# Performance work log

Hardware: AMD Instinct MI355X
Metric: run time of the kernel (lower is better)

Reference implementation:

```python
import jax, jax.numpy as jnp
import numpy as np

B, DIN, DOUT = 8192, 4096, 4096
BIAS_OFFSET = 512.0


def setup_inputs() -> dict:
    key = jax.random.key(0)
    kx, kw = jax.random.split(key)
    x = jax.random.normal(kx, (B, DIN), dtype=jnp.float32)
    # Ternary weights in {-1, 0, 1}, iid with zero_prob=0.5 and mean 0:
    # P(0)=0.5, P(-1)=P(1)=0.25
    u = jax.random.uniform(kw, (DIN, DOUT))
    W = jnp.where(u < 0.25, -1.0, jnp.where(u < 0.5, 1.0, 0.0)).astype(jnp.float32)
    b = jnp.full((DOUT,), BIAS_OFFSET, dtype=jnp.float32)
    return {"x": x, "W": W, "b": b}


def reference(x, W, b):
    # z: pre-activation of ternary-weight linear layer  [B, DOUT]
    z = jnp.matmul(x, W) + b
    # binarized activation (sign with ties -> +1), as in TernBin forward
    x_out = jnp.where(z >= 0, 1.0, -1.0).astype(z.dtype)
    return (x_out, z)
```

## Files before the change

### kernel.cpp

```cpp
#include <hip/hip_runtime.h>
#include <stdint.h>

#define MDIM 8192
#define NDIM 4096
#define KDIM 4096

#define BM 256
#define BN 256
#define BK 64
#define NT (KDIM / BK)

#define CVT_X_BLOCKS 16384
#define CVT_W_BLOCKS 4096

typedef __bf16 bf16x8 __attribute__((ext_vector_type(8)));
typedef float f32x4 __attribute__((ext_vector_type(4)));

#define GPTR(p) ((const __attribute__((address_space(1))) void*)(p))
#define LPTR(p) ((__attribute__((address_space(3))) void*)(p))

#define BAR() asm volatile("s_barrier" ::: "memory")

__device__ __forceinline__ uint32_t f2bf(float f) {
  union { float f; uint32_t u; } c; c.f = f;
  uint32_t u = c.u;
  u += 0x7fffu + ((u >> 16) & 1u);
  return u >> 16;
}

__global__ __launch_bounds__(256) void cvt_fused(const float* __restrict__ x,
                                                 const float* __restrict__ W,
                                                 unsigned short* __restrict__ xb,
                                                 unsigned short* __restrict__ Wt) {
  __shared__ uint32_t T[64][37];
  const int bid = blockIdx.x;
  const int t = threadIdx.x;
  if (bid < CVT_X_BLOCKS) {
    size_t i = ((size_t)bid * 256 + t) * 8;
    const float4* p = (const float4*)(x + i);
    float4 a = p[0], b = p[1];
    uint4 r;
    r.x = f2bf(a.x) | (f2bf(a.y) << 16);
    r.y = f2bf(a.z) | (f2bf(a.w) << 16);
    r.z = f2bf(b.x) | (f2bf(b.y) << 16);
    r.w = f2bf(b.z) | (f2bf(b.w) << 16);
    *(uint4*)(xb + i) = r;
  } else {
    const int wb = bid - CVT_X_BLOCKS;
    const int n0 = (wb & 63) * 64;
    const int k0 = (wb >> 6) * 64;
    const int nl = t & 63;
    const int kpb = t >> 6;
#pragma unroll
    for (int i = 0; i < 8; ++i) {
      int kp = kpb + 4 * i;
      int k = 2 * kp;
      float v0 = W[(size_t)(k0 + k) * NDIM + n0 + nl];
      float v1 = W[(size_t)(k0 + k + 1) * NDIM + n0 + nl];
      T[nl][kp] = f2bf(v0) | (f2bf(v1) << 16);
    }
    __syncthreads();
    const int ch = t & 7;
    const int nb = t >> 3;
#pragma unroll
    for (int h = 0; h < 2; ++h) {
      int n = nb + 32 * h;
      uint4 v;
      v.x = T[n][ch * 4 + 0];
      v.y = T[n][ch * 4 + 1];
      v.z = T[n][ch * 4 + 2];
      v.w = T[n][ch * 4 + 3];
      *(uint4*)&Wt[(size_t)(n0 + n) * KDIM + k0 + ch * 8] = v;
    }
  }
}


__device__ __forceinline__ void stage2(unsigned short* dst,
                                       const unsigned short* G, int half,
                                       int tile, int wave) {
#pragma unroll
  for (int i = 0; i < 2; ++i) {
    const int rb = half * 128 + i * 64;
    __builtin_amdgcn_global_load_lds(
        GPTR(G + (size_t)rb * KDIM + (size_t)tile * 64),
        LPTR(dst + (rb + wave * 8) * BK), 16, 0, 0);
  }
}

template <int IB>
__device__ __forceinline__ void load_a4(const unsigned short* buf, int wm,
                                        int rA, int k0off, int k1off,
                                        bf16x8 (&a)[4][2]) {
#pragma unroll
  for (int i = 0; i < 4; ++i) {
    const unsigned short* p = buf + (size_t)(wm * 128 + (IB + i) * 16 + rA) * BK;
    a[i][0] = *(const bf16x8*)(p + k0off);
    a[i][1] = *(const bf16x8*)(p + k1off);
  }
}

template <int JB>
__device__ __forceinline__ void load_b2(const unsigned short* buf, int wn,
                                        int rA, int k0off, int k1off,
                                        bf16x8 (&b)[4][2]) {
#pragma unroll
  for (int j = 0; j < 2; ++j) {
    const unsigned short* p = buf + (size_t)(wn * 64 + (JB + j) * 16 + rA) * BK;
    b[JB + j][0] = *(const bf16x8*)(p + k0off);
    b[JB + j][1] = *(const bf16x8*)(p + k1off);
  }
}

template <int IB, int JB>
__device__ __forceinline__ void mfma16(const bf16x8 (&a)[4][2],
                                       const bf16x8 (&b)[4][2],
                                       f32x4 (&acc)[8][4]) {
  __builtin_amdgcn_s_setprio(1);
#pragma unroll
  for (int i = 0; i < 4; ++i)
#pragma unroll
    for (int j = 0; j < 2; ++j)
#pragma unroll
      for (int kk = 0; kk < 2; ++kk)
        acc[IB + i][JB + j] = __builtin_amdgcn_mfma_f32_16x16x32_bf16(
            b[JB + j][kk], a[i][kk], acc[IB + i][JB + j], 0, 0, 0);
  __builtin_amdgcn_s_setprio(0);
}

template <bool SA, bool SB, int VM>
__device__ __forceinline__ void tile_step(
    const unsigned short* curA, const unsigned short* curB,
    unsigned short* nxtA, unsigned short* stageB, int T,
    const unsigned short* Ag, const unsigned short* Bg, int wave, int wm,
    int wn, int rA, int k0off, int k1off, bf16x8 (&a)[4][2], bf16x8 (&b)[4][2],
    f32x4 (&acc)[8][4]) {
  load_a4<0>(curA, wm, rA, k0off, k1off, a);
  load_b2<0>(curB, wn, rA, k0off, k1off, b);
  if (SA) stage2(nxtA, Ag, 0, T + 1, wave);
  BAR();
  mfma16<0, 0>(a, b, acc);
  BAR();
  load_b2<2>(curB, wn, rA, k0off, k1off, b);
  if (SA) stage2(nxtA, Ag, 1, T + 1, wave);
  BAR();
  mfma16<0, 2>(a, b, acc);
  BAR();
  load_a4<4>(curA, wm, rA, k0off, k1off, a);
  if (SB) stage2(stageB, Bg, 0, T + 2, wave);
  BAR();
  mfma16<4, 0>(a, b, acc);
  BAR();
  if (SB) stage2(stageB, Bg, 1, T + 2, wave);
  if constexpr (VM == 4) asm volatile("s_waitcnt vmcnt(4)" ::: "memory");
  else if constexpr (VM == 0) asm volatile("s_waitcnt vmcnt(0)" ::: "memory");
  BAR();
  mfma16<4, 2>(a, b, acc);
  BAR();
}

__global__ __launch_bounds__(512, 2) void gemm_bf16_8ph(
    const unsigned short* __restrict__ Ab, const unsigned short* __restrict__ Bt,
    const float* __restrict__ bias, float* __restrict__ out) {
  __shared__ __align__(16) unsigned short lds[4 * BM * BK];
  unsigned short* A0 = lds;
  unsigned short* B0 = lds + 1 * BM * BK;
  unsigned short* A1 = lds + 2 * BM * BK;
  unsigned short* B1 = lds + 3 * BM * BK;

  const int tid = threadIdx.x;
  const int lane = tid & 63;
  const int wave = tid >> 6;
  const int wm = wave & 1;
  const int wn = wave >> 1;

  const int bid = blockIdx.x;
  const int wg = (bid & 7) * 64 + (bid >> 3);
  const int m0 = (wg >> 4) * BM;
  const int n0 = (wg & 15) * BN;

  f32x4 acc[8][4];
#pragma unroll
  for (int i = 0; i < 8; ++i)
#pragma unroll
    for (int j = 0; j < 4; ++j) {
      f32x4 z = {0.0f, 0.0f, 0.0f, 0.0f};
      acc[i][j] = z;
    }

  const int tr = tid >> 3;
  const int tc = (tid & 7) ^ (tr & 7);
  const unsigned short* Ag = Ab + (size_t)(m0 + tr) * KDIM + tc * 8;
  const unsigned short* Bg = Bt + (size_t)(n0 + tr) * KDIM + tc * 8;

  const int rA = lane & 15;
  const int hi = lane >> 4;
  const int key = lane & 7;
  const int k0off = ((0 + hi) ^ key) * 8;
  const int k1off = ((4 + hi) ^ key) * 8;

  bf16x8 a[4][2], b[4][2];

  stage2(B0, Bg, 0, 0, wave);
  stage2(B0, Bg, 1, 0, wave);
  stage2(A0, Ag, 0, 0, wave);
  stage2(A0, Ag, 1, 0, wave);
  stage2(B1, Bg, 0, 1, wave);
  stage2(B1, Bg, 1, 1, wave);
  asm volatile("s_waitcnt vmcnt(4)" ::: "memory");
  BAR();

  for (int T = 0; T < NT - 2; T += 2) {
    tile_step<true, true, 4>(A0, B0, A1, B0, T, Ag, Bg, wave, wm, wn, rA,
                             k0off, k1off, a, b, acc);
    tile_step<true, true, 4>(A1, B1, A0, B1, T + 1, Ag, Bg, wave, wm, wn, rA,
                             k0off, k1off, a, b, acc);
  }
  tile_step<true, false, 0>(A0, B0, A1, B0, NT - 2, Ag, Bg, wave, wm, wn, rA,
                            k0off, k1off, a, b, acc);
  tile_step<false, false, -1>(A1, B1, A0, B1, NT - 1, Ag, Bg, wave, wm, wn, rA,
                              k0off, k1off, a, b, acc);

  float* zout = out + (size_t)MDIM * NDIM;
  const int ml = lane & 15;
  const int nb4 = (lane >> 4) * 4;
#pragma unroll
  for (int i = 0; i < 8; ++i) {
    int m = m0 + wm * 128 + i * 16 + ml;
    float* zrow = zout + (size_t)m * NDIM;
    float* srow = out + (size_t)m * NDIM;
#pragma unroll
    for (int j = 0; j < 4; ++j) {
      int n = n0 + wn * 64 + j * 16 + nb4;
      float4 bv = *(const float4*)&bias[n];
      f32x4 v = acc[i][j];
      float4 z, s;
      z.x = v[0] + bv.x; z.y = v[1] + bv.y; z.z = v[2] + bv.z; z.w = v[3] + bv.w;
      s.x = (z.x >= 0.0f) ? 1.0f : -1.0f;
      s.y = (z.y >= 0.0f) ? 1.0f : -1.0f;
      s.z = (z.z >= 0.0f) ? 1.0f : -1.0f;
      s.w = (z.w >= 0.0f) ? 1.0f : -1.0f;
      *(float4*)&zrow[n] = z;
      *(float4*)&srow[n] = s;
    }
  }
}

__device__ __forceinline__ void mfma_step128(const unsigned short* As,
                                             const unsigned short* Bs,
                                             f32x4 acc[4][4], int lane, int wm,
                                             int wn) {
  const int rA = lane & 15;
  const int key = lane & 7;
#pragma unroll
  for (int kk = 0; kk < 2; ++kk) {
    const int koff = ((kk * 4 + (lane >> 4)) ^ key) * 8;
    bf16x8 a[4], b[4];
#pragma unroll
    for (int i = 0; i < 4; ++i) {
      a[i] = *(const bf16x8*)(As + (size_t)(wm * 64 + i * 16 + rA) * 64 + koff);
      b[i] = *(const bf16x8*)(Bs + (size_t)(wn * 64 + i * 16 + rA) * 64 + koff);
    }
#pragma unroll
    for (int i = 0; i < 4; ++i)
#pragma unroll
      for (int j = 0; j < 4; ++j)
        acc[i][j] = __builtin_amdgcn_mfma_f32_16x16x32_bf16(b[j], a[i],
                                                            acc[i][j], 0, 0, 0);
  }
}

__global__ __launch_bounds__(256) void gemm_bf16_nows(
    const float* __restrict__ x, const float* __restrict__ W,
    const float* __restrict__ bias, float* __restrict__ out) {
  __shared__ __align__(16) unsigned short As[128 * 64];
  __shared__ __align__(16) unsigned short Bs[128 * 64];

  const int tid = threadIdx.x;
  const int lane = tid & 63;
  const int wave = tid >> 6;
  const int wm = wave & 1;
  const int wn = wave >> 1;
  const int m0 = blockIdx.y * 128;
  const int n0 = blockIdx.x * 128;

  f32x4 acc[4][4];
#pragma unroll
  for (int i = 0; i < 4; ++i)
#pragma unroll
    for (int j = 0; j < 4; ++j) {
      f32x4 z = {0.0f, 0.0f, 0.0f, 0.0f};
      acc[i][j] = z;
    }

  for (int k0 = 0; k0 < KDIM; k0 += 64) {
    {
      const int kc = (tid & 15) * 4;
      const int cb = kc >> 3;
      const int wi = kc & 7;
      const int rowb = tid >> 4;
#pragma unroll
      for (int r = 0; r < 8; ++r) {
        int row = rowb + 16 * r;
        float4 v = *(const float4*)&x[(size_t)(m0 + row) * KDIM + k0 + kc];
        uint2 pk;
        pk.x = f2bf(v.x) | (f2bf(v.y) << 16);
        pk.y = f2bf(v.z) | (f2bf(v.w) << 16);
        *(uint2*)&As[row * 64 + ((cb ^ (row & 7)) * 8) + wi] = pk;
      }
    }
    {
      const int nc = (tid & 31) * 4;
      const int kb = tid >> 5;
#pragma unroll
      for (int r = 0; r < 8; ++r) {
        int krow = kb + 8 * r;
        int cb = krow >> 3, wi = krow & 7;
        float4 v = *(const float4*)&W[(size_t)(k0 + krow) * NDIM + n0 + nc];
        Bs[(nc + 0) * 64 + ((cb ^ ((nc + 0) & 7)) * 8) + wi] = (unsigned short)f2bf(v.x);
        Bs[(nc + 1) * 64 + ((cb ^ ((nc + 1) & 7)) * 8) + wi] = (unsigned short)f2bf(v.y);
        Bs[(nc + 2) * 64 + ((cb ^ ((nc + 2) & 7)) * 8) + wi] = (unsigned short)f2bf(v.z);
        Bs[(nc + 3) * 64 + ((cb ^ ((nc + 3) & 7)) * 8) + wi] = (unsigned short)f2bf(v.w);
      }
    }
    __syncthreads();
    mfma_step128(As, Bs, acc, lane, wm, wn);
    __syncthreads();
  }

  float* zout = out + (size_t)MDIM * NDIM;
  const int ml = lane & 15;
  const int nb4 = (lane >> 4) * 4;
#pragma unroll
  for (int i = 0; i < 4; ++i) {
    int m = m0 + wm * 64 + i * 16 + ml;
    float* zrow = zout + (size_t)m * NDIM;
    float* srow = out + (size_t)m * NDIM;
#pragma unroll
    for (int j = 0; j < 4; ++j) {
      int n = n0 + wn * 64 + j * 16 + nb4;
      float4 bv = *(const float4*)&bias[n];
      f32x4 v = acc[i][j];
      float4 z, s;
      z.x = v[0] + bv.x; z.y = v[1] + bv.y; z.z = v[2] + bv.z; z.w = v[3] + bv.w;
      s.x = (z.x >= 0.0f) ? 1.0f : -1.0f;
      s.y = (z.y >= 0.0f) ? 1.0f : -1.0f;
      s.z = (z.z >= 0.0f) ? 1.0f : -1.0f;
      s.w = (z.w >= 0.0f) ? 1.0f : -1.0f;
      *(float4*)&zrow[n] = z;
      *(float4*)&srow[n] = s;
    }
  }
}

extern "C" void kernel_launch(void* const* d_in, const int* in_sizes, int n_in,
                              void* d_out, int out_size, void* d_ws,
                              size_t ws_size, hipStream_t stream) {
  (void)in_sizes; (void)n_in; (void)out_size;
  const float* x = (const float*)d_in[0];
  const float* W = (const float*)d_in[1];
  const float* b = (const float*)d_in[2];
  float* out = (float*)d_out;

  const size_t xb_elems = (size_t)MDIM * KDIM;
  const size_t wt_elems = (size_t)KDIM * NDIM;
  const size_t need = (xb_elems + wt_elems) * sizeof(unsigned short);

  if (ws_size >= need) {
    unsigned short* xb = (unsigned short*)d_ws;
    unsigned short* wt = xb + xb_elems;
    cvt_fused<<<CVT_X_BLOCKS + CVT_W_BLOCKS, 256, 0, stream>>>(x, W, xb, wt);
    gemm_bf16_8ph<<<(MDIM / BM) * (NDIM / BN), 512, 0, stream>>>(xb, wt, b, out);
  } else {
    dim3 fgrid(NDIM / 128, MDIM / 128);
    gemm_bf16_nows<<<fgrid, 256, 0, stream>>>(x, W, b, out);
  }
}
```

Measured before the change: 602.2 us.

## Fuse fp32-to-bf16 conversion of x into GEMM A-tile loading

Drops the separate pass that converted x to bf16 in workspace. The GEMM now loads fp32 x into registers, converts it with packed bf16 conversion instructions, and writes swizzled tiles to LDS within the pipeline. This removes the pre-pass write and re-read of a 64MB intermediate. In exchange, the GEMM reads fp32 A, which doubles the A bytes per tile, and holds extra staging registers.

Result: slower. 778.2 us (+29.2%).

```diff
diff --git a/kernel.cpp b/kernel.cpp
--- a/kernel.cpp
+++ b/kernel.cpp
@@ -10,7 +10,6 @@
 #define BK 64
 #define NT (KDIM / BK)
 
-#define CVT_X_BLOCKS 16384
 #define CVT_W_BLOCKS 4096
 
 typedef __bf16 bf16x8 __attribute__((ext_vector_type(8)));
@@ -28,50 +27,41 @@
   return u >> 16;
 }
 
-__global__ __launch_bounds__(256) void cvt_fused(const float* __restrict__ x,
-                                                 const float* __restrict__ W,
-                                                 unsigned short* __restrict__ xb,
-                                                 unsigned short* __restrict__ Wt) {
+__device__ __forceinline__ uint32_t cvtpk(float lo, float hi) {
+  uint32_t r;
+  asm("v_cvt_pk_bf16_f32 %0, %1, %2" : "=v"(r) : "v"(lo), "v"(hi));
+  return r;
+}
+
+__global__ __launch_bounds__(256) void cvt_w(const float* __restrict__ W,
+                                             unsigned short* __restrict__ Wt) {
   __shared__ uint32_t T[64][37];
-  const int bid = blockIdx.x;
+  const int wb = blockIdx.x;
   const int t = threadIdx.x;
-  if (bid < CVT_X_BLOCKS) {
-    size_t i = ((size_t)bid * 256 + t) * 8;
-    const float4* p = (const float4*)(x + i);
-    float4 a = p[0], b = p[1];
-    uint4 r;
-    r.x = f2bf(a.x) | (f2bf(a.y) << 16);
-    r.y = f2bf(a.z) | (f2bf(a.w) << 16);
-    r.z = f2bf(b.x) | (f2bf(b.y) << 16);
-    r.w = f2bf(b.z) | (f2bf(b.w) << 16);
-    *(uint4*)(xb + i) = r;
-  } else {
-    const int wb = bid - CVT_X_BLOCKS;
-    const int n0 = (wb & 63) * 64;
-    const int k0 = (wb >> 6) * 64;
-    const int nl = t & 63;
-    const int kpb = t >> 6;
-#pragma unroll
-    for (int i = 0; i < 8; ++i) {
-      int kp = kpb + 4 * i;
-      int k = 2 * kp;
-      float v0 = W[(size_t)(k0 + k) * NDIM + n0 + nl];
-      float v1 = W[(size_t)(k0 + k + 1) * NDIM + n0 + nl];
-      T[nl][kp] = f2bf(v0) | (f2bf(v1) << 16);
-    }
-    __syncthreads();
-    const int ch = t & 7;
-    const int nb = t >> 3;
-#pragma unroll
-    for (int h = 0; h < 2; ++h) {
-      int n = nb + 32 * h;
-      uint4 v;
-      v.x = T[n][ch * 4 + 0];
-      v.y = T[n][ch * 4 + 1];
-      v.z = T[n][ch * 4 + 2];
-      v.w = T[n][ch * 4 + 3];
-      *(uint4*)&Wt[(size_t)(n0 + n) * KDIM + k0 + ch * 8] = v;
-    }
+  const int n0 = (wb & 63) * 64;
+  const int k0 = (wb >> 6) * 64;
+  const int nl = t & 63;
+  const int kpb = t >> 6;
+#pragma unroll
+  for (int i = 0; i < 8; ++i) {
+    int kp = kpb + 4 * i;
+    int k = 2 * kp;
+    float v0 = W[(size_t)(k0 + k) * NDIM + n0 + nl];
+    float v1 = W[(size_t)(k0 + k + 1) * NDIM + n0 + nl];
+    T[nl][kp] = f2bf(v0) | (f2bf(v1) << 16);
+  }
+  __syncthreads();
+  const int ch = t & 7;
+  const int nb = t >> 3;
+#pragma unroll
+  for (int h = 0; h < 2; ++h) {
+    int n = nb + 32 * h;
+    uint4 v;
+    v.x = T[n][ch * 4 + 0];
+    v.y = T[n][ch * 4 + 1];
+    v.z = T[n][ch * 4 + 2];
+    v.w = T[n][ch * 4 + 3];
+    *(uint4*)&Wt[(size_t)(n0 + n) * KDIM + k0 + ch * 8] = v;
   }
 }
 
@@ -88,6 +78,30 @@
   }
 }
 
+template <int C0>
+__device__ __forceinline__ void issueA2(const float* const (&aptr)[4], int kf,
+                                        float4 (&areg)[4][2]) {
+#pragma unroll
+  for (int c = C0; c < C0 + 2; ++c) {
+    areg[c][0] = *(const float4*)(aptr[c] + kf);
+    areg[c][1] = *(const float4*)(aptr[c] + kf + 4);
+  }
+}
+
+__device__ __forceinline__ void writeA(unsigned short* nxtA,
+                                       const int (&alds)[4],
+                                       const float4 (&areg)[4][2]) {
+#pragma unroll
+  for (int c = 0; c < 4; ++c) {
+    uint4 v;
+    v.x = cvtpk(areg[c][0].x, areg[c][0].y);
+    v.y = cvtpk(areg[c][0].z, areg[c][0].w);
+    v.z = cvtpk(areg[c][1].x, areg[c][1].y);
+    v.w = cvtpk(areg[c][1].z, areg[c][1].w);
+    *(uint4*)(nxtA + alds[c]) = v;
+  }
+}
+
 template <int IB>
 __device__ __forceinline__ void load_a4(const unsigned short* buf, int wm,
                                         int rA, int k0off, int k1off,
@@ -132,17 +146,19 @@
 __device__ __forceinline__ void tile_step(
     const unsigned short* curA, const unsigned short* curB,
     unsigned short* nxtA, unsigned short* stageB, int T,
-    const unsigned short* Ag, const unsigned short* Bg, int wave, int wm,
-    int wn, int rA, int k0off, int k1off, bf16x8 (&a)[4][2], bf16x8 (&b)[4][2],
+    const float* const (&aptr)[4], const int (&alds)[4],
+    float4 (&areg)[4][2], const unsigned short* Bg, int wave, int wm, int wn,
+    int rA, int k0off, int k1off, bf16x8 (&a)[4][2], bf16x8 (&b)[4][2],
     f32x4 (&acc)[8][4]) {
+  const int kf = (T + 1) * BK;
   load_a4<0>(curA, wm, rA, k0off, k1off, a);
   load_b2<0>(curB, wn, rA, k0off, k1off, b);
-  if (SA) stage2(nxtA, Ag, 0, T + 1, wave);
+  if (SA) issueA2<0>(aptr, kf, areg);
   BAR();
   mfma16<0, 0>(a, b, acc);
   BAR();
   load_b2<2>(curB, wn, rA, k0off, k1off, b);
-  if (SA) stage2(nxtA, Ag, 1, T + 1, wave);
+  if (SA) issueA2<2>(aptr, kf, areg);
   BAR();
   mfma16<0, 2>(a, b, acc);
   BAR();
@@ -154,13 +170,15 @@
   if (SB) stage2(stageB, Bg, 1, T + 2, wave);
   if constexpr (VM == 4) asm volatile("s_waitcnt vmcnt(4)" ::: "memory");
   else if constexpr (VM == 0) asm volatile("s_waitcnt vmcnt(0)" ::: "memory");
+  if (SA) writeA(nxtA, alds, areg);
   BAR();
   mfma16<4, 2>(a, b, acc);
+  if (SA) asm volatile("s_waitcnt lgkmcnt(0)" ::: "memory");
   BAR();
 }
 
 __global__ __launch_bounds__(512, 2) void gemm_bf16_8ph(
-    const unsigned short* __restrict__ Ab, const unsigned short* __restrict__ Bt,
+    const float* __restrict__ x, const unsigned short* __restrict__ Bt,
     const float* __restrict__ bias, float* __restrict__ out) {
   __shared__ __align__(16) unsigned short lds[4 * BM * BK];
   unsigned short* A0 = lds;
@@ -190,8 +208,17 @@
 
   const int tr = tid >> 3;
   const int tc = (tid & 7) ^ (tr & 7);
-  const unsigned short* Ag = Ab + (size_t)(m0 + tr) * KDIM + tc * 8;
   const unsigned short* Bg = Bt + (size_t)(n0 + tr) * KDIM + tc * 8;
+
+  const float* aptr[4];
+  int alds[4];
+#pragma unroll
+  for (int c = 0; c < 4; ++c) {
+    const int r = (2 * wave + (c >> 1)) * 16 + (lane & 15);
+    const int u = (c & 1) * 4 + (lane >> 4);
+    aptr[c] = x + (size_t)(m0 + r) * KDIM + u * 8;
+    alds[c] = r * BK + (u ^ (lane & 7)) * 8;
+  }
 
   const int rA = lane & 15;
   const int hi = lane >> 4;
@@ -200,26 +227,29 @@
   const int k1off = ((4 + hi) ^ key) * 8;
 
   bf16x8 a[4][2], b[4][2];
-
+  float4 areg[4][2];
+
+  issueA2<0>(aptr, 0, areg);
+  issueA2<2>(aptr, 0, areg);
   stage2(B0, Bg, 0, 0, wave);
   stage2(B0, Bg, 1, 0, wave);
-  stage2(A0, Ag, 0, 0, wave);
-  stage2(A0, Ag, 1, 0, wave);
   stage2(B1, Bg, 0, 1, wave);
   stage2(B1, Bg, 1, 1, wave);
   asm volatile("s_waitcnt vmcnt(4)" ::: "memory");
+  writeA(A0, alds, areg);
+  asm volatile("s_waitcnt lgkmcnt(0)" ::: "memory");
   BAR();
 
   for (int T = 0; T < NT - 2; T += 2) {
-    tile_step<true, true, 4>(A0, B0, A1, B0, T, Ag, Bg, wave, wm, wn, rA,
-                             k0off, k1off, a, b, acc);
-    tile_step<true, true, 4>(A1, B1, A0, B1, T + 1, Ag, Bg, wave, wm, wn, rA,
-                             k0off, k1off, a, b, acc);
-  }
-  tile_step<true, false, 0>(A0, B0, A1, B0, NT - 2, Ag, Bg, wave, wm, wn, rA,
-                            k0off, k1off, a, b, acc);
-  tile_step<false, false, -1>(A1, B1, A0, B1, NT - 1, Ag, Bg, wave, wm, wn, rA,
-                              k0off, k1off, a, b, acc);
+    tile_step<true, true, 4>(A0, B0, A1, B0, T, aptr, alds, areg, Bg, wave,
+                             wm, wn, rA, k0off, k1off, a, b, acc);
+    tile_step<true, true, 4>(A1, B1, A0, B1, T + 1, aptr, alds, areg, Bg,
+                             wave, wm, wn, rA, k0off, k1off, a, b, acc);
+  }
+  tile_step<true, false, 0>(A0, B0, A1, B0, NT - 2, aptr, alds, areg, Bg,
+                            wave, wm, wn, rA, k0off, k1off, a, b, acc);
+  tile_step<false, false, -1>(A1, B1, A0, B1, NT - 1, aptr, alds, areg, Bg,
+                              wave, wm, wn, rA, k0off, k1off, a, b, acc);
 
   float* zout = out + (size_t)MDIM * NDIM;
   const int ml = lane & 15;
@@ -362,15 +392,13 @@
   const float* b = (const float*)d_in[2];
   float* out = (float*)d_out;
 
-  const size_t xb_elems = (size_t)MDIM * KDIM;
   const size_t wt_elems = (size_t)KDIM * NDIM;
-  const size_t need = (xb_elems + wt_elems) * sizeof(unsigned short);
+  const size_t need = wt_elems * sizeof(unsigned short);
 
   if (ws_size >= need) {
-    unsigned short* xb = (unsigned short*)d_ws;
-    unsigned short* wt = xb + xb_elems;
-    cvt_fused<<<CVT_X_BLOCKS + CVT_W_BLOCKS, 256, 0, stream>>>(x, W, xb, wt);
-    gemm_bf16_8ph<<<(MDIM / BM) * (NDIM / BN), 512, 0, stream>>>(xb, wt, b, out);
+    unsigned short* wt = (unsigned short*)d_ws;
+    cvt_w<<<CVT_W_BLOCKS, 256, 0, stream>>>(W, wt);
+    gemm_bf16_8ph<<<(MDIM / BM) * (NDIM / BN), 512, 0, stream>>>(x, wt, b, out);
   } else {
     dim3 fgrid(NDIM / 128, MDIM / 128);
     gemm_bf16_nows<<<fgrid, 256, 0, stream>>>(x, W, b, out);
```

## Prefetch A and B two tiles ahead with unified staging schedule

Applied to the files above, without the earlier changes.

Changes the global-to-LDS prefetch so A is loaded two K-tiles ahead, like B, instead of one tile ahead. Both A and B are now staged into the buffer currently being consumed, during the second half of each tile step, once its first-half reads are done. The row-half mapping in stage2 is reordered so each half covers rows that have already been read. The goal is deeper latency hiding for A loads, at the cost of more loads in flight, with the wait count raised from 4 to 8 to match.

Result: slower. 625.6 us (+3.9%).

```diff
diff --git a/kernel.cpp b/kernel.cpp
--- a/kernel.cpp
+++ b/kernel.cpp
@@ -81,7 +81,7 @@
                                        int tile, int wave) {
 #pragma unroll
   for (int i = 0; i < 2; ++i) {
-    const int rb = half * 128 + i * 64;
+    const int rb = i * 128 + half * 64;
     __builtin_amdgcn_global_load_lds(
         GPTR(G + (size_t)rb * KDIM + (size_t)tile * 64),
         LPTR(dst + (rb + wave * 8) * BK), 16, 0, 0);
@@ -128,31 +128,34 @@
   __builtin_amdgcn_s_setprio(0);
 }
 
-template <bool SA, bool SB, int VM>
+template <bool S, int VM>
 __device__ __forceinline__ void tile_step(
-    const unsigned short* curA, const unsigned short* curB,
-    unsigned short* nxtA, unsigned short* stageB, int T,
+    unsigned short* curA, unsigned short* curB, int T,
     const unsigned short* Ag, const unsigned short* Bg, int wave, int wm,
     int wn, int rA, int k0off, int k1off, bf16x8 (&a)[4][2], bf16x8 (&b)[4][2],
     f32x4 (&acc)[8][4]) {
   load_a4<0>(curA, wm, rA, k0off, k1off, a);
   load_b2<0>(curB, wn, rA, k0off, k1off, b);
-  if (SA) stage2(nxtA, Ag, 0, T + 1, wave);
   BAR();
   mfma16<0, 0>(a, b, acc);
   BAR();
   load_b2<2>(curB, wn, rA, k0off, k1off, b);
-  if (SA) stage2(nxtA, Ag, 1, T + 1, wave);
   BAR();
   mfma16<0, 2>(a, b, acc);
   BAR();
   load_a4<4>(curA, wm, rA, k0off, k1off, a);
-  if (SB) stage2(stageB, Bg, 0, T + 2, wave);
+  if (S) {
+    stage2(curB, Bg, 0, T + 2, wave);
+    stage2(curA, Ag, 0, T + 2, wave);
+  }
   BAR();
   mfma16<4, 0>(a, b, acc);
   BAR();
-  if (SB) stage2(stageB, Bg, 1, T + 2, wave);
-  if constexpr (VM == 4) asm volatile("s_waitcnt vmcnt(4)" ::: "memory");
+  if (S) {
+    stage2(curB, Bg, 1, T + 2, wave);
+    stage2(curA, Ag, 1, T + 2, wave);
+  }
+  if constexpr (VM == 8) asm volatile("s_waitcnt vmcnt(8)" ::: "memory");
   else if constexpr (VM == 0) asm volatile("s_waitcnt vmcnt(0)" ::: "memory");
   BAR();
   mfma16<4, 2>(a, b, acc);
@@ -202,24 +205,26 @@
   bf16x8 a[4][2], b[4][2];
 
   stage2(B0, Bg, 0, 0, wave);
+  stage2(A0, Ag, 0, 0, wave);
   stage2(B0, Bg, 1, 0, wave);
-  stage2(A0, Ag, 0, 0, wave);
   stage2(A0, Ag, 1, 0, wave);
   stage2(B1, Bg, 0, 1, wave);
+  stage2(A1, Ag, 0, 1, wave);
   stage2(B1, Bg, 1, 1, wave);
-  asm volatile("s_waitcnt vmcnt(4)" ::: "memory");
+  stage2(A1, Ag, 1, 1, wave);
+  asm volatile("s_waitcnt vmcnt(8)" ::: "memory");
   BAR();
 
   for (int T = 0; T < NT - 2; T += 2) {
-    tile_step<true, true, 4>(A0, B0, A1, B0, T, Ag, Bg, wave, wm, wn, rA,
-                             k0off, k1off, a, b, acc);
-    tile_step<true, true, 4>(A1, B1, A0, B1, T + 1, Ag, Bg, wave, wm, wn, rA,
-                             k0off, k1off, a, b, acc);
-  }
-  tile_step<true, false, 0>(A0, B0, A1, B0, NT - 2, Ag, Bg, wave, wm, wn, rA,
-                            k0off, k1off, a, b, acc);
-  tile_step<false, false, -1>(A1, B1, A0, B1, NT - 1, Ag, Bg, wave, wm, wn, rA,
-                              k0off, k1off, a, b, acc);
+    tile_step<true, 8>(A0, B0, T, Ag, Bg, wave, wm, wn, rA, k0off, k1off, a,
+                       b, acc);
+    tile_step<true, 8>(A1, B1, T + 1, Ag, Bg, wave, wm, wn, rA, k0off, k1off,
+                       a, b, acc);
+  }
+  tile_step<false, 0>(A0, B0, NT - 2, Ag, Bg, wave, wm, wn, rA, k0off, k1off,
+                      a, b, acc);
+  tile_step<false, -1>(A1, B1, NT - 1, Ag, Bg, wave, wm, wn, rA, k0off, k1off,
+                       a, b, acc);
 
   float* zout = out + (size_t)MDIM * NDIM;
   const int ml = lane & 15;
```
